# Kernel optimization log

Hardware: AMD Instinct MI355X
Metric: run time of the kernel (lower is better)

The kernel has to match this reference:

```python
import jax, jax.numpy as jnp
import numpy as np

B, N, H, A, S = 8, 8192, 256, 64, 32  # batch, nodes, hidden, annotation, sub_graphs


def _mysoftmax(x):
    # exp, zero out where x <= 0, normalize over last dim, nan (0/0) -> 0
    x_exp = jnp.where(x > 0, jnp.exp(x), 0.0)
    part = jnp.sum(x_exp, axis=-1, keepdims=True)
    # safe divide: where partition == 0 the faithful result after nan_to_num is 0
    return jnp.where(part > 0, x_exp / jnp.where(part > 0, part, 1.0), 0.0)


def setup_inputs() -> dict:
    key = jax.random.key(0)
    k1, k2, k3, k4, k5, k6 = jax.random.split(key, 6)
    x = jax.random.normal(k1, (B, N, H + A), dtype=jnp.float32)
    node_map = jax.random.uniform(k2, (B, S, N), dtype=jnp.float32)
    lim = 1.0 / np.sqrt(H + A)
    Wi = jax.random.uniform(k3, (H, H + A), minval=-lim, maxval=lim, dtype=jnp.float32)
    bi = jax.random.uniform(k4, (H,), minval=-lim, maxval=lim, dtype=jnp.float32)
    Wj = jax.random.uniform(k5, (H, H + A), minval=-lim, maxval=lim, dtype=jnp.float32)
    bj = jax.random.uniform(k6, (H,), minval=-lim, maxval=lim, dtype=jnp.float32)
    return {"x": x, "node_map": node_map, "Wi": Wi, "bi": bi, "Wj": Wj, "bj": bj}


def reference(x, node_map, Wi, bi, Wj, bj):
    # gated node features: sigmoid(fc_i(x)) * tanh(fc_j(x))  -> [B, N, H]
    x_sigm = jax.nn.sigmoid(jnp.einsum('bnf,hf->bnh', x, Wi) + bi)
    x_tanh = jnp.tanh(jnp.einsum('bnf,hf->bnh', x, Wj) + bj)
    x_all = x_sigm * x_tanh
    # per-node L2 norm -> [B, 1, N]
    x_norm = jnp.linalg.norm(x_all, axis=-1)[:, None, :]
    # scaled subgraph map and masked softmax over nodes -> [B, S, N]
    weight = _mysoftmax(node_map * x_norm)
    # weighted sum over nodes (replaces [B,S,N,H] broadcast) -> [B, S, H]
    pooled = jnp.einsum('bsn,bnh->bsh', weight, x_all)
    return jnp.tanh(pooled), weight[..., None]
```

## Files before the change

### kernel.cpp

```cpp
#include <hip/hip_runtime.h>
#include <cstdint>
#include <cstddef>

typedef unsigned short u16;
typedef unsigned int   u32;
using short8 = __attribute__((ext_vector_type(8))) short;
using f32x4  = __attribute__((ext_vector_type(4))) float;

#define NB    8
#define NN    8192
#define HH    256
#define FF    320
#define SS    32
#define NROWS 65536
#define NCH   32

__device__ __forceinline__ u16 f2bf(float f) {
    union { float f; u32 u; } v; v.f = f;
    u32 r = v.u + 0x7fffu + ((v.u >> 16) & 1u);
    return (u16)(r >> 16);
}
__device__ __forceinline__ u32 pk2(float lo, float hi) {
    u32 r;
    asm("v_cvt_pk_bf16_f32 %0, %1, %2" : "=v"(r) : "v"(lo), "v"(hi));
    return r;
}
__device__ __forceinline__ short8 pack8(float4 a, float4 b) {
    union { u32 u[4]; short8 s; } r;
    r.u[0] = pk2(a.x, a.y); r.u[1] = pk2(a.z, a.w);
    r.u[2] = pk2(b.x, b.y); r.u[3] = pk2(b.z, b.w);
    return r.s;
}

__global__ __launch_bounds__(256) void prep_w(const float* __restrict__ Wi,
                                              const float* __restrict__ Wj,
                                              u16* __restrict__ Wb,
                                              float* __restrict__ normsq) {
    int idx = blockIdx.x * 256 + threadIdx.x;
    float v = (idx < 81920) ? Wi[idx] : Wj[idx - 81920];
    Wb[idx] = f2bf(v);
    if (idx < NROWS) normsq[idx] = 0.f;
}

__global__ __launch_bounds__(512, 3) void gemm_gate(
    const float* __restrict__ x, const u16* __restrict__ Wb,
    const float* __restrict__ bi, const float* __restrict__ bj,
    u16* __restrict__ xa, float* __restrict__ normsq)
{
    __shared__ u16 lB[5 * 8192];

    const int bx   = blockIdx.x;
    const int xcd  = bx & 7;
    const int ht   = (bx >> 3) & 3;
    const int slot = bx >> 5;
    const int mb   = xcd + slot * 8;
    const int m0   = mb * 256;
    const int h0   = ht * 64;
    const int b_idx = m0 >> 13;
    const int n0    = m0 & 8191;

    const int tid  = threadIdx.x;
    const int w    = tid >> 6;
    const int lane = tid & 63;
    const int quad = lane >> 4;
    const int l15  = lane & 15;

    {
        const int rsub = lane >> 3;
        const int kg   = (lane & 7) ^ rsub;
        #pragma unroll
        for (int kt = 0; kt < 5; ++kt) {
            #pragma unroll
            for (int j = 0; j < 2; ++j) {
                int sl  = w * 2 + j;
                int row = sl * 8 + rsub;
                int mat = row >> 6, hl = row & 63;
                const u16* gsrc = Wb + mat * 81920 + (size_t)(h0 + hl) * FF + kt * 64 + kg * 8;
                u16* ldst = &lB[kt * 8192 + sl * 512];
                __builtin_amdgcn_global_load_lds(
                    (const __attribute__((address_space(1))) void*)gsrc,
                    (__attribute__((address_space(3))) void*)ldst, 16, 0, 0);
            }
        }
    }

    const float* xb = x + (size_t)(m0 + w * 32 + l15) * FF + quad * 8;

    f32x4 acc[8][2];
    #pragma unroll
    for (int a = 0; a < 8; ++a)
        #pragma unroll
        for (int m = 0; m < 2; ++m) acc[a][m] = (f32x4){0.f, 0.f, 0.f, 0.f};

    float4 pre[4][2][2];
    #pragma unroll
    for (int p = 0; p < 3; ++p)
        #pragma unroll
        for (int mt = 0; mt < 2; ++mt) {
            pre[p][mt][0] = *reinterpret_cast<const float4*>(xb + mt * 16 * FF + p * 32);
            pre[p][mt][1] = *reinterpret_cast<const float4*>(xb + mt * 16 * FF + p * 32 + 4);
        }

    __syncthreads();

    #pragma unroll
    for (int ks = 0; ks < 10; ++ks) {
        const int cur = ks & 3;
        if (ks < 7) {
            const int nxt = (ks + 3) & 3;
            const int f   = (ks + 3) * 32;
            #pragma unroll
            for (int mt = 0; mt < 2; ++mt) {
                pre[nxt][mt][0] = *reinterpret_cast<const float4*>(xb + mt * 16 * FF + f);
                pre[nxt][mt][1] = *reinterpret_cast<const float4*>(xb + mt * 16 * FF + f + 4);
            }
        }
        __builtin_amdgcn_sched_barrier(0);
        short8 af[2];
        #pragma unroll
        for (int mt = 0; mt < 2; ++mt)
            af[mt] = pack8(pre[cur][mt][0], pre[cur][mt][1]);
        const int kt = ks >> 1, kk = ks & 1;
        #pragma unroll
        for (int mn = 0; mn < 8; ++mn) {
            int c = mn * 16 + l15;
            short8 bv = *reinterpret_cast<const short8*>(
                &lB[kt * 8192 + c * 64 + (((kk * 4 + quad) ^ (c & 7)) << 3)]);
            acc[mn][0] = __builtin_amdgcn_mfma_f32_16x16x32_bf16(af[0], bv, acc[mn][0], 0, 0, 0);
            acc[mn][1] = __builtin_amdgcn_mfma_f32_16x16x32_bf16(af[1], bv, acc[mn][1], 0, 0, 0);
        }
    }

    float s0[2][4];
    #pragma unroll
    for (int mt = 0; mt < 2; ++mt)
        #pragma unroll
        for (int r = 0; r < 4; ++r) s0[mt][r] = 0.f;

    #pragma unroll
    for (int hq = 0; hq < 4; ++hq) {
        int h = h0 + hq * 16 + l15;
        float bi_v = bi[h], bj_v = bj[h];
        #pragma unroll
        for (int mt = 0; mt < 2; ++mt) {
            float xall[4];
            #pragma unroll
            for (int r = 0; r < 4; ++r) {
                float yi = acc[hq][mt][r] + bi_v;
                float yj = acc[hq + 4][mt][r] + bj_v;
                float sg = 1.f / (1.f + __expf(-yi));
                float e2 = __expf(-2.f * yj);
                float th = (1.f - e2) / (1.f + e2);
                float xv = sg * th;
                xall[r] = xv;
                s0[mt][r] += xv * xv;
            }
            uint2 pk;
            pk.x = pk2(xall[0], xall[1]);
            pk.y = pk2(xall[2], xall[3]);
            size_t o = (size_t)b_idx * ((size_t)HH * NN) + (size_t)h * NN
                     + (size_t)(n0 + w * 32 + mt * 16 + quad * 4);
            *reinterpret_cast<uint2*>(&xa[o]) = pk;
        }
    }
    #pragma unroll
    for (int m = 1; m <= 8; m <<= 1) {
        #pragma unroll
        for (int mt = 0; mt < 2; ++mt)
            #pragma unroll
            for (int r = 0; r < 4; ++r)
                s0[mt][r] += __shfl_xor(s0[mt][r], m, 64);
    }
    if (l15 == 0) {
        #pragma unroll
        for (int mt = 0; mt < 2; ++mt)
            #pragma unroll
            for (int r = 0; r < 4; ++r)
                atomicAdd(&normsq[m0 + w * 32 + mt * 16 + quad * 4 + r], s0[mt][r]);
    }
}

__global__ __launch_bounds__(1024) void softmax_k(
    const float* __restrict__ nm, const float* __restrict__ normsq,
    float* __restrict__ out1)
{
    __shared__ float red[16];
    int bs = blockIdx.x;
    int b  = bs >> 5;
    const float* src = nm + (size_t)bs * NN;
    float* dst       = out1 + (size_t)bs * NN;
    const float* ns  = normsq + (size_t)b * NN;
    int tid = threadIdx.x;
    float e[8];
    float sum = 0.f;
    #pragma unroll
    for (int i = 0; i < 8; ++i) {
        int n = i * 1024 + tid;
        float logit = src[n] * sqrtf(ns[n]);
        float v = (logit > 0.f) ? __expf(logit) : 0.f;
        e[i] = v;
        sum += v;
    }
    #pragma unroll
    for (int m = 1; m <= 32; m <<= 1) sum += __shfl_xor(sum, m, 64);
    int w = tid >> 6, lane = tid & 63;
    if (lane == 0) red[w] = sum;
    __syncthreads();
    float part = 0.f;
    #pragma unroll
    for (int j = 0; j < 16; ++j) part += red[j];
    float inv = (part > 0.f) ? (1.f / part) : 0.f;
    #pragma unroll
    for (int i = 0; i < 8; ++i) dst[i * 1024 + tid] = e[i] * inv;
}

__global__ __launch_bounds__(256) void pooled_k(
    const u16* __restrict__ xa, const float* __restrict__ wgt,
    float* __restrict__ part)
{
    __shared__ u16 lx[4 * 4096];
    __shared__ u16 lw[32 * 264];
    int bx = blockIdx.x;
    int ht = bx >> 8;
    int bc = bx & 255;
    int b  = bc >> 5, c = bc & 31;
    int n0 = c * 256;
    int tid = threadIdx.x, w = tid >> 6, lane = tid & 63, quad = lane >> 4, l15 = lane & 15;

    {
        const int rsub = lane >> 3;
        const int kg   = (lane & 7) ^ rsub;
        const u16* xbase = xa + (size_t)b * ((size_t)HH * NN)
                         + (size_t)(ht * 64) * NN + n0;
        #pragma unroll
        for (int nt = 0; nt < 4; ++nt) {
            #pragma unroll
            for (int j = 0; j < 2; ++j) {
                int sl  = w * 2 + j;
                int row = sl * 8 + rsub;
                const u16* gsrc = xbase + (size_t)row * NN + nt * 64 + kg * 8;
                u16* ldst = &lx[nt * 4096 + sl * 512];
                __builtin_amdgcn_global_load_lds(
                    (const __attribute__((address_space(1))) void*)gsrc,
                    (__attribute__((address_space(3))) void*)ldst, 16, 0, 0);
            }
        }
    }

    {
        int s  = tid >> 3;
        int nb = (tid & 7) * 32;
        const float* src = wgt + (size_t)(b * SS + s) * NN + n0 + nb;
        #pragma unroll
        for (int q = 0; q < 8; ++q) {
            float4 v = *reinterpret_cast<const float4*>(src + q * 4);
            uint2 pk;
            pk.x = pk2(v.x, v.y);
            pk.y = pk2(v.z, v.w);
            *reinterpret_cast<uint2*>(&lw[s * 264 + nb + q * 4]) = pk;
        }
    }
    __syncthreads();

    f32x4 acc[2];
    acc[0] = (f32x4){0.f, 0.f, 0.f, 0.f};
    acc[1] = (f32x4){0.f, 0.f, 0.f, 0.f};

    const int r = w * 16 + l15;
    #pragma unroll
    for (int ks = 0; ks < 8; ++ks) {
        const int nt = ks >> 1;
        const int g  = (ks & 1) * 4 + quad;
        short8 av = *reinterpret_cast<const short8*>(
            &lx[nt * 4096 + (r >> 3) * 512 + (r & 7) * 64 + ((g ^ (r & 7)) << 3)]);
        #pragma unroll
        for (int st = 0; st < 2; ++st) {
            int s = st * 16 + l15;
            short8 bv = *reinterpret_cast<const short8*>(&lw[s * 264 + ks * 32 + quad * 8]);
            acc[st] = __builtin_amdgcn_mfma_f32_16x16x32_bf16(av, bv, acc[st], 0, 0, 0);
        }
    }
    float* pb = part + (size_t)(b * NCH + c) * 8192;
    #pragma unroll
    for (int st = 0; st < 2; ++st) {
        int h = ht * 64 + w * 16 + quad * 4;
        int s = st * 16 + l15;
        *reinterpret_cast<f32x4*>(&pb[s * 256 + h]) = acc[st];
    }
}

__global__ __launch_bounds__(256) void reduce_tanh(const float* __restrict__ part,
                                                   float* __restrict__ out0)
{
    int gid = blockIdx.x * 256 + threadIdx.x;
    int b = gid >> 13, r = gid & 8191;
    const float* p = part + (size_t)b * NCH * 8192 + r;
    float s = 0.f;
    #pragma unroll
    for (int c = 0; c < NCH; ++c) s += p[(size_t)c * 8192];
    out0[gid] = tanhf(s);
}

extern "C" void kernel_launch(void* const* d_in, const int* in_sizes, int n_in,
                              void* d_out, int out_size, void* d_ws, size_t ws_size,
                              hipStream_t stream) {
    const float* x  = (const float*)d_in[0];
    const float* nm = (const float*)d_in[1];
    const float* Wi = (const float*)d_in[2];
    const float* bi = (const float*)d_in[3];
    const float* Wj = (const float*)d_in[4];
    const float* bj = (const float*)d_in[5];
    float* out0 = (float*)d_out;
    float* out1 = out0 + NB * SS * HH;

    char* ws = (char*)d_ws;
    u16*   Wb     = (u16*)ws;
    u16*   xa     = (u16*)(ws + 327680);
    float* normsq = (float*)(ws + 327680 + 33554432);
    float* part   = (float*)(ws + 327680 + 33554432 + 262144);

    prep_w     <<<640,  256, 0, stream>>>(Wi, Wj, Wb, normsq);
    gemm_gate  <<<1024, 512, 0, stream>>>(x, Wb, bi, bj, xa, normsq);
    softmax_k  <<<256, 1024, 0, stream>>>(nm, normsq, out1);
    pooled_k   <<<1024, 256, 0, stream>>>(xa, out1, part);
    reduce_tanh<<<256,  256, 0, stream>>>(part, out0);
}
```

Baseline: 197.1 us.

## Stage x tiles via async global-to-LDS loads with double buffering in gate GEMM

The gate GEMM now loads fp32 x tiles directly into LDS with global_load_lds, using a swizzled layout, instead of prefetching them into registers. The Wb slices are streamed per k-step through a double-buffered LDS ring rather than loaded in full up front. Blocks shrink to 256 threads with each wave covering 64 rows (4 m-tiles), which raises B-fragment reuse per wave. The aim is to overlap memory with MFMA work and cut register pressure, at the cost of an 80KB LDS footprint, a barrier per k-step and lower occupancy.

```diff
diff --git a/kernel.cpp b/kernel.cpp
--- a/kernel.cpp
+++ b/kernel.cpp
@@ -14,6 +14,9 @@
 #define SS    32
 #define NROWS 65536
 #define NCH   32
+
+#define AS1 __attribute__((address_space(1)))
+#define AS3 __attribute__((address_space(3)))
 
 __device__ __forceinline__ u16 f2bf(float f) {
     union { float f; u32 u; } v; v.f = f;
@@ -42,12 +45,12 @@
     if (idx < NROWS) normsq[idx] = 0.f;
 }
 
-__global__ __launch_bounds__(512, 3) void gemm_gate(
+__global__ __launch_bounds__(256, 2) void gemm_gate(
     const float* __restrict__ x, const u16* __restrict__ Wb,
     const float* __restrict__ bi, const float* __restrict__ bj,
     u16* __restrict__ xa, float* __restrict__ normsq)
 {
-    __shared__ u16 lB[5 * 8192];
+    __shared__ char lds[81920];
 
     const int bx   = blockIdx.x;
     const int xcd  = bx & 7;
@@ -65,75 +68,73 @@
     const int quad = lane >> 4;
     const int l15  = lane & 15;
 
-    {
-        const int rsub = lane >> 3;
-        const int kg   = (lane & 7) ^ rsub;
-        #pragma unroll
-        for (int kt = 0; kt < 5; ++kt) {
-            #pragma unroll
-            for (int j = 0; j < 2; ++j) {
-                int sl  = w * 2 + j;
-                int row = sl * 8 + rsub;
-                int mat = row >> 6, hl = row & 63;
-                const u16* gsrc = Wb + mat * 81920 + (size_t)(h0 + hl) * FF + kt * 64 + kg * 8;
-                u16* ldst = &lB[kt * 8192 + sl * 512];
-                __builtin_amdgcn_global_load_lds(
-                    (const __attribute__((address_space(1))) void*)gsrc,
-                    (__attribute__((address_space(3))) void*)ldst, 16, 0, 0);
-            }
-        }
-    }
-
-    const float* xb = x + (size_t)(m0 + w * 32 + l15) * FF + quad * 8;
-
-    f32x4 acc[8][2];
+    char* lA = lds;
+    char* lB = lds + 65536;
+
+    const int arow = lane >> 3;
+    const float* srcA0 = x + (size_t)(m0 + w * 64 + arow) * FF
+                       + ((lane & 7) ^ arow) * 4;
+    const int bg  = (((lane & 3) ^ ((lane >> 3) & 3)) << 3);
+    const int bcl = lane >> 2;
+
+    f32x4 acc[8][4];
     #pragma unroll
     for (int a = 0; a < 8; ++a)
         #pragma unroll
-        for (int m = 0; m < 2; ++m) acc[a][m] = (f32x4){0.f, 0.f, 0.f, 0.f};
-
-    float4 pre[4][2][2];
-    #pragma unroll
-    for (int p = 0; p < 3; ++p)
-        #pragma unroll
-        for (int mt = 0; mt < 2; ++mt) {
-            pre[p][mt][0] = *reinterpret_cast<const float4*>(xb + mt * 16 * FF + p * 32);
-            pre[p][mt][1] = *reinterpret_cast<const float4*>(xb + mt * 16 * FF + p * 32 + 4);
-        }
-
+        for (int m = 0; m < 4; ++m) acc[a][m] = (f32x4){0.f, 0.f, 0.f, 0.f};
+
+    auto stage = [&](int ks, int buf) {
+        #pragma unroll
+        for (int j = 0; j < 8; ++j) {
+            const float* gsrc = srcA0 + (size_t)j * 8 * FF + ks * 32;
+            char* ldst = lA + buf * 32768 + (w * 8 + j) * 1024;
+            __builtin_amdgcn_global_load_lds(
+                (const AS1 void*)gsrc, (AS3 void*)ldst, 16, 0, 0);
+        }
+        #pragma unroll
+        for (int j = 0; j < 2; ++j) {
+            int c   = (w * 2 + j) * 16 + bcl;
+            int mat = c >> 6, hl = c & 63;
+            const u16* gsrc = Wb + mat * 81920 + (size_t)(h0 + hl) * FF + ks * 32 + bg;
+            char* ldst = lB + buf * 8192 + (w * 2 + j) * 1024;
+            __builtin_amdgcn_global_load_lds(
+                (const AS1 void*)gsrc, (AS3 void*)ldst, 16, 0, 0);
+        }
+    };
+
+    stage(0, 0);
     __syncthreads();
 
     #pragma unroll
     for (int ks = 0; ks < 10; ++ks) {
-        const int cur = ks & 3;
-        if (ks < 7) {
-            const int nxt = (ks + 3) & 3;
-            const int f   = (ks + 3) * 32;
-            #pragma unroll
-            for (int mt = 0; mt < 2; ++mt) {
-                pre[nxt][mt][0] = *reinterpret_cast<const float4*>(xb + mt * 16 * FF + f);
-                pre[nxt][mt][1] = *reinterpret_cast<const float4*>(xb + mt * 16 * FF + f + 4);
-            }
-        }
+        const int cur = ks & 1;
+        if (ks < 9) stage(ks + 1, cur ^ 1);
         __builtin_amdgcn_sched_barrier(0);
-        short8 af[2];
-        #pragma unroll
-        for (int mt = 0; mt < 2; ++mt)
-            af[mt] = pack8(pre[cur][mt][0], pre[cur][mt][1]);
-        const int kt = ks >> 1, kk = ks & 1;
+
+        short8 af[4];
+        #pragma unroll
+        for (int mt = 0; mt < 4; ++mt) {
+            const int r = w * 64 + mt * 16 + l15;
+            const char* base = lA + cur * 32768 + r * 128;
+            float4 lo = *reinterpret_cast<const float4*>(base + (((2 * quad    ) ^ (l15 & 7)) << 4));
+            float4 hi = *reinterpret_cast<const float4*>(base + (((2 * quad + 1) ^ (l15 & 7)) << 4));
+            af[mt] = pack8(lo, hi);
+        }
         #pragma unroll
         for (int mn = 0; mn < 8; ++mn) {
-            int c = mn * 16 + l15;
+            const int c = mn * 16 + l15;
             short8 bv = *reinterpret_cast<const short8*>(
-                &lB[kt * 8192 + c * 64 + (((kk * 4 + quad) ^ (c & 7)) << 3)]);
-            acc[mn][0] = __builtin_amdgcn_mfma_f32_16x16x32_bf16(af[0], bv, acc[mn][0], 0, 0, 0);
-            acc[mn][1] = __builtin_amdgcn_mfma_f32_16x16x32_bf16(af[1], bv, acc[mn][1], 0, 0, 0);
-        }
-    }
-
-    float s0[2][4];
-    #pragma unroll
-    for (int mt = 0; mt < 2; ++mt)
+                lB + cur * 8192 + c * 64 + ((quad ^ ((l15 >> 1) & 3)) << 4));
+            #pragma unroll
+            for (int mt = 0; mt < 4; ++mt)
+                acc[mn][mt] = __builtin_amdgcn_mfma_f32_16x16x32_bf16(af[mt], bv, acc[mn][mt], 0, 0, 0);
+        }
+        __syncthreads();
+    }
+
+    float s0[4][4];
+    #pragma unroll
+    for (int mt = 0; mt < 4; ++mt)
         #pragma unroll
         for (int r = 0; r < 4; ++r) s0[mt][r] = 0.f;
 
@@ -142,7 +143,7 @@
         int h = h0 + hq * 16 + l15;
         float bi_v = bi[h], bj_v = bj[h];
         #pragma unroll
-        for (int mt = 0; mt < 2; ++mt) {
+        for (int mt = 0; mt < 4; ++mt) {
             float xall[4];
             #pragma unroll
             for (int r = 0; r < 4; ++r) {
@@ -159,24 +160,24 @@
             pk.x = pk2(xall[0], xall[1]);
             pk.y = pk2(xall[2], xall[3]);
             size_t o = (size_t)b_idx * ((size_t)HH * NN) + (size_t)h * NN
-                     + (size_t)(n0 + w * 32 + mt * 16 + quad * 4);
+                     + (size_t)(n0 + w * 64 + mt * 16 + quad * 4);
             *reinterpret_cast<uint2*>(&xa[o]) = pk;
         }
     }
     #pragma unroll
     for (int m = 1; m <= 8; m <<= 1) {
         #pragma unroll
-        for (int mt = 0; mt < 2; ++mt)
+        for (int mt = 0; mt < 4; ++mt)
             #pragma unroll
             for (int r = 0; r < 4; ++r)
                 s0[mt][r] += __shfl_xor(s0[mt][r], m, 64);
     }
     if (l15 == 0) {
         #pragma unroll
-        for (int mt = 0; mt < 2; ++mt)
+        for (int mt = 0; mt < 4; ++mt)
             #pragma unroll
             for (int r = 0; r < 4; ++r)
-                atomicAdd(&normsq[m0 + w * 32 + mt * 16 + quad * 4 + r], s0[mt][r]);
+                atomicAdd(&normsq[m0 + w * 64 + mt * 16 + quad * 4 + r], s0[mt][r]);
     }
 }
 
@@ -241,8 +242,7 @@
                 const u16* gsrc = xbase + (size_t)row * NN + nt * 64 + kg * 8;
                 u16* ldst = &lx[nt * 4096 + sl * 512];
                 __builtin_amdgcn_global_load_lds(
-                    (const __attribute__((address_space(1))) void*)gsrc,
-                    (__attribute__((address_space(3))) void*)ldst, 16, 0, 0);
+                    (const AS1 void*)gsrc, (AS3 void*)ldst, 16, 0, 0);
             }
         }
     }
@@ -320,7 +320,7 @@
     float* part   = (float*)(ws + 327680 + 33554432 + 262144);
 
     prep_w     <<<640,  256, 0, stream>>>(Wi, Wj, Wb, normsq);
-    gemm_gate  <<<1024, 512, 0, stream>>>(x, Wb, bi, bj, xa, normsq);
+    gemm_gate  <<<1024, 256, 0, stream>>>(x, Wb, bi, bj, xa, normsq);
     softmax_k  <<<256, 1024, 0, stream>>>(nm, normsq, out1);
     pooled_k   <<<1024, 256, 0, stream>>>(xa, out1, part);
     reduce_tanh<<<256,  256, 0, stream>>>(part, out0);
```

New measurement: 200.6 us. Within noise of the previous version (+1.8%).
